# Optimization experiments

Hardware: AMD Instinct MI355X
Metric: run time of the kernel (lower is better)

## Reference

```python
import jax, jax.numpy as jnp
import numpy as np

V, E, H, L, B, T = 371, 512, 8, 8, 4, 1024
D = E // H
EPS = 1e-5


def setup_inputs() -> dict:
    key = jax.random.key(0)
    ks = jax.random.split(key, 7)
    s = 0.02
    return {
        "idx": jax.random.randint(ks[0], (B, T), 0, V),
        "wte": jax.random.normal(ks[1], (V, E), jnp.float32) * s,   # tied with lm_head
        "wpe": jax.random.normal(ks[2], (T, E), jnp.float32) * s,
        "c_attn_w": jax.random.normal(ks[3], (L, E, 3 * E), jnp.float32) * s,
        "c_proj_w": jax.random.normal(ks[4], (L, E, E), jnp.float32) * s,
        "fc_w": jax.random.normal(ks[5], (L, E, 4 * E), jnp.float32) * s,
        "fc_proj_w": jax.random.normal(ks[6], (L, 4 * E, E), jnp.float32) * s,
        "ln1_w": jnp.ones((L, E), jnp.float32),
        "ln2_w": jnp.ones((L, E), jnp.float32),
        "lnf_w": jnp.ones((E,), jnp.float32),
    }


def _ln(x, w):
    m = jnp.mean(x, axis=-1, keepdims=True)
    v = jnp.mean((x - m) ** 2, axis=-1, keepdims=True)
    return (x - m) * jax.lax.rsqrt(v + EPS) * w


def reference(idx, wte, wpe, c_attn_w, c_proj_w, fc_w, fc_proj_w, ln1_w, ln2_w, lnf_w):
    mask = jnp.tril(jnp.ones((T, T), bool))  # causal mask, as in the registered buffer
    scale = 1.0 / np.sqrt(D)

    x0 = wte[idx] + wpe[None, :T]  # [B,T,E]

    def block(x, p):
        aw, pw, l1, l2, fw, fpw = p
        h = _ln(x, l1)
        qkv = h @ aw                                   # [B,T,3E]
        q, k, v = jnp.split(qkv, 3, axis=-1)
        q = q.reshape(B, T, H, D)
        k = k.reshape(B, T, H, D)
        v = v.reshape(B, T, H, D)
        att = jnp.einsum("bqhd,bkhd->bhqk", q, k) * scale  # full TxT scores (faithful)
        att = jnp.where(mask[None, None], att, -jnp.inf)
        att = jax.nn.softmax(att, axis=-1)
        y = jnp.einsum("bhqk,bkhd->bqhd", att, v).reshape(B, T, E)
        x = x + y @ pw
        h = _ln(x, l2)
        x = x + jax.nn.gelu(h @ fw, approximate=False) @ fpw
        return x, None

    x, _ = jax.lax.scan(block, x0, (c_attn_w, c_proj_w, ln1_w, ln2_w, fc_w, fc_proj_w))
    x = _ln(x, lnf_w)
    logits = x @ wte.T  # weight tying: lm_head.weight = wte.weight
    return logits
```

## Files before the change

### kernel.cpp

```cpp
#include <hip/hip_runtime.h>


#define VOCAB 371
#define VPAD  384
#define EMB   512
#define NH    8
#define NL    8
#define TS    1024
#define NTOK  4096
#define NEG_INF (-1e30f)

typedef unsigned short ushort_t;
typedef __attribute__((ext_vector_type(8))) short short8;
typedef __attribute__((ext_vector_type(4))) float f32x4;

__device__ inline float bf2f(ushort_t b) {
    unsigned int u = ((unsigned int)b) << 16;
    float f; __builtin_memcpy(&f, &u, 4); return f;
}
__device__ inline ushort_t f2bf(float f) {
    unsigned int u; __builtin_memcpy(&u, &f, 4);
    u = (u + 0x7fff + ((u >> 16) & 1)) >> 16;
    return (ushort_t)u;
}

__global__ __launch_bounds__(64) void detect_k(const ushort_t* __restrict__ w,
        int* __restrict__ flag)
{
    int i = threadIdx.x;
    float v = bf2f(w[2 * i]);
    bool ok = (__builtin_fabsf(v) <= 4.0f);
    unsigned long long m = __ballot(ok);
    if (i == 0) flag[0] = (__popcll(m) >= 56) ? 1 : 0;
}

__global__ __launch_bounds__(256) void sentinel_k(ushort_t* __restrict__ out, int n)
{
    int i = blockIdx.x * 256 + threadIdx.x;
    if (i < n) out[i] = 0x447A;
}

__global__ __launch_bounds__(256) void embed_k(const int* __restrict__ idx,
        const void* __restrict__ wte, const void* __restrict__ wpe,
        float* __restrict__ x, const int* __restrict__ flag)
{
    int n = blockIdx.x, tid = threadIdx.x;
    int t = n & (TS - 1);
    int v = idx[n];
    size_t o = (size_t)n * EMB;
    float a0, a1, b0, b1;
    if (*flag) {
        const ushort_t* te = (const ushort_t*)wte; const ushort_t* pe = (const ushort_t*)wpe;
        a0 = bf2f(te[v * EMB + tid]); a1 = bf2f(te[v * EMB + 256 + tid]);
        b0 = bf2f(pe[t * EMB + tid]); b1 = bf2f(pe[t * EMB + 256 + tid]);
    } else {
        const float* te = (const float*)wte; const float* pe = (const float*)wpe;
        a0 = te[v * EMB + tid]; a1 = te[v * EMB + 256 + tid];
        b0 = pe[t * EMB + tid]; b1 = pe[t * EMB + 256 + tid];
    }
    x[o + tid] = a0 + b0;
    x[o + 256 + tid] = a1 + b1;
}

__global__ __launch_bounds__(256) void ln_k(const float* __restrict__ x,
        const void* __restrict__ w, long woff, ushort_t* __restrict__ out,
        const int* __restrict__ flag)
{
    const int row = blockIdx.x * 4 + (threadIdx.x >> 6);
    const int lane = threadIdx.x & 63;
    const float* xr = x + (size_t)row * EMB + lane * 8;
    float4 f0 = *(const float4*)xr;
    float4 f1 = *(const float4*)(xr + 4);
    float v[8] = {f0.x, f0.y, f0.z, f0.w, f1.x, f1.y, f1.z, f1.w};
    float s = ((v[0] + v[1]) + (v[2] + v[3])) + ((v[4] + v[5]) + (v[6] + v[7]));
#pragma unroll
    for (int off = 32; off > 0; off >>= 1) s += __shfl_xor(s, off, 64);
    float mean = s * (1.0f / EMB);
    float s2 = 0.f;
#pragma unroll
    for (int j = 0; j < 8; ++j) { v[j] -= mean; s2 += v[j] * v[j]; }
#pragma unroll
    for (int off = 32; off > 0; off >>= 1) s2 += __shfl_xor(s2, off, 64);
    float rs = rsqrtf(s2 * (1.0f / EMB) + 1e-5f);
    float g[8];
    if (*flag) {
        const ushort_t* wb = (const ushort_t*)w + woff + lane * 8;
        ushort_t tmp[8];
        *(uint4*)tmp = *(const uint4*)wb;
#pragma unroll
        for (int j = 0; j < 8; ++j) g[j] = bf2f(tmp[j]);
    } else {
        const float* wf = (const float*)w + woff + lane * 8;
        float4 g0 = *(const float4*)wf;
        float4 g1 = *(const float4*)(wf + 4);
        g[0] = g0.x; g[1] = g0.y; g[2] = g0.z; g[3] = g0.w;
        g[4] = g1.x; g[5] = g1.y; g[6] = g1.z; g[7] = g1.w;
    }
    ushort_t ob[8];
#pragma unroll
    for (int j = 0; j < 8; ++j) ob[j] = f2bf(v[j] * rs * g[j]);
    *(uint4*)(out + (size_t)row * EMB + lane * 8) = *(uint4*)ob;
}

__global__ __launch_bounds__(256) void wtrans_k(const void* __restrict__ aw,
        const void* __restrict__ pw, const void* __restrict__ fw,
        const void* __restrict__ fpw, long l, ushort_t* __restrict__ wbuf,
        const int* __restrict__ flag)
{
    __shared__ float tile[64][65];
    const int isbf = *flag;
    long lay = (l < 0) ? (long)blockIdx.z : l;
    ushort_t* obase = wbuf + ((l < 0) ? (size_t)blockIdx.z * 3145728 : 0);
    int t = blockIdx.x;
    const void* src; ushort_t* dst; int Kw, Nw; long ioff;
    if (t < 192)      { src = aw;  dst = obase;           Kw = 512;  Nw = 1536; ioff = lay * 512L * 1536; }
    else if (t < 256) { t -= 192; src = pw;  dst = obase + 786432;  Kw = 512;  Nw = 512;  ioff = lay * 512L * 512; }
    else if (t < 512) { t -= 256; src = fw;  dst = obase + 1048576; Kw = 512;  Nw = 2048; ioff = lay * 512L * 2048; }
    else              { t -= 512; src = fpw; dst = obase + 2097152; Kw = 2048; Nw = 512;  ioff = lay * 2048L * 512; }
    int tn = Nw >> 6;
    int n0 = (t % tn) * 64, k0 = (t / tn) * 64;
    const int r = threadIdx.x >> 2, cq = (threadIdx.x & 3) * 16;
    size_t ii = ioff + (size_t)(k0 + r) * Nw + n0 + cq;
    if (isbf) {
        const ushort_t* sb = (const ushort_t*)src + ii;
        ushort_t tmp[16];
        *(uint4*)tmp = *(const uint4*)sb;
        *(uint4*)(tmp + 8) = *(const uint4*)(sb + 8);
#pragma unroll
        for (int j = 0; j < 16; ++j) tile[r][cq + j] = bf2f(tmp[j]);
    } else {
        const float* sf = (const float*)src + ii;
        *(float4*)&tile[r][cq]      = *(const float4*)sf;
        *(float4*)&tile[r][cq + 4]  = *(const float4*)(sf + 4);
        *(float4*)&tile[r][cq + 8]  = *(const float4*)(sf + 8);
        *(float4*)&tile[r][cq + 12] = *(const float4*)(sf + 12);
    }
    __syncthreads();
    const int kc = (threadIdx.x & 7) * 8;
#pragma unroll
    for (int j = 0; j < 2; ++j) {
        const int n = (threadIdx.x >> 3) + j * 32;
        unsigned pk[4];
#pragma unroll
        for (int i = 0; i < 4; ++i) {
            unsigned lo = f2bf(tile[kc + 2 * i][n]);
            unsigned hi = f2bf(tile[kc + 2 * i + 1][n]);
            pk[i] = lo | (hi << 16);
        }
        *(uint4*)(dst + (size_t)(n0 + n) * Kw + k0 + kc) = *(uint4*)pk;
    }
}

__global__ __launch_bounds__(256) void wconv_k(const void* __restrict__ in,
        ushort_t* __restrict__ out, int n, int nreal, const int* __restrict__ flag)
{
    int i = blockIdx.x * 256 + threadIdx.x;
    if (i >= n) return;
    ushort_t v = 0;
    if (i < nreal) v = (*flag) ? ((const ushort_t*)in)[i] : f2bf(((const float*)in)[i]);
    out[i] = v;
}

__global__ __launch_bounds__(256) void gemm_wide(const ushort_t* __restrict__ A,
        const ushort_t* __restrict__ Bt, int M, int N, int K,
        float* __restrict__ outF, ushort_t* __restrict__ outB,
        const float* __restrict__ res, int act)
{
    __shared__ ushort_t Al[128 * 72];
    __shared__ ushort_t Bl[64 * 72];
    const int tid = threadIdx.x;
    const int wave = tid >> 6, lane = tid & 63;
    const int quad = lane >> 4, l16 = lane & 15;
    const int m0 = blockIdx.y * 128, n0 = blockIdx.x * 64;
    const int ar = tid >> 1, ac = (tid & 1) * 32;
    const int br = tid >> 2, bc = (tid & 3) * 16;
    const ushort_t* Ag = A + (size_t)(m0 + ar) * K + ac;
    const ushort_t* Bg = Bt + (size_t)(n0 + br) * K + bc;
    f32x4 acc[2][4] = {};
    uint4 a0 = *(const uint4*)(Ag);
    uint4 a1 = *(const uint4*)(Ag + 8);
    uint4 a2 = *(const uint4*)(Ag + 16);
    uint4 a3 = *(const uint4*)(Ag + 24);
    uint4 b0 = *(const uint4*)(Bg);
    uint4 b1 = *(const uint4*)(Bg + 8);
    for (int k0 = 0; k0 < K; k0 += 64) {
        __syncthreads();
        *(uint4*)&Al[ar * 72 + ac]      = a0;
        *(uint4*)&Al[ar * 72 + ac + 8]  = a1;
        *(uint4*)&Al[ar * 72 + ac + 16] = a2;
        *(uint4*)&Al[ar * 72 + ac + 24] = a3;
        *(uint4*)&Bl[br * 72 + bc]     = b0;
        *(uint4*)&Bl[br * 72 + bc + 8] = b1;
        __syncthreads();
        if (k0 + 64 < K) {
            a0 = *(const uint4*)(Ag + k0 + 64);
            a1 = *(const uint4*)(Ag + k0 + 72);
            a2 = *(const uint4*)(Ag + k0 + 80);
            a3 = *(const uint4*)(Ag + k0 + 88);
            b0 = *(const uint4*)(Bg + k0 + 64);
            b1 = *(const uint4*)(Bg + k0 + 72);
        }
#pragma unroll
        for (int ks = 0; ks < 2; ++ks) {
            short8 af[2], bf[4];
#pragma unroll
            for (int mi = 0; mi < 2; ++mi)
                af[mi] = *(const short8*)&Al[(wave * 32 + mi * 16 + l16) * 72 + ks * 32 + quad * 8];
#pragma unroll
            for (int ni = 0; ni < 4; ++ni)
                bf[ni] = *(const short8*)&Bl[(ni * 16 + l16) * 72 + ks * 32 + quad * 8];
#pragma unroll
            for (int mi = 0; mi < 2; ++mi)
#pragma unroll
                for (int ni = 0; ni < 4; ++ni)
                    acc[mi][ni] = __builtin_amdgcn_mfma_f32_16x16x32_bf16(
                            af[mi], bf[ni], acc[mi][ni], 0, 0, 0);
        }
    }
#pragma unroll
    for (int mi = 0; mi < 2; ++mi) {
        const int rowb = m0 + wave * 32 + mi * 16 + quad * 4;
#pragma unroll
        for (int ni = 0; ni < 4; ++ni) {
            const int col = n0 + ni * 16 + l16;
#pragma unroll
            for (int r = 0; r < 4; ++r) {
                size_t o = (size_t)(rowb + r) * N + col;
                float v = acc[mi][ni][r];
                if (res) v += res[o];
                if (act) v = 0.5f * v * (1.0f + erff(v * 0.70710678118f));
                if (outF) outF[o] = v;
                else      outB[o] = f2bf(v);
            }
        }
    }
}

__global__ __launch_bounds__(256) void gemm_nt(const ushort_t* __restrict__ A,
        const ushort_t* __restrict__ Bt, int M, int N, int K,
        float* __restrict__ outF, ushort_t* __restrict__ outB, void* __restrict__ outD,
        const float* __restrict__ res, int act, const int* __restrict__ flag)
{
    __shared__ ushort_t Al[64 * 72];
    __shared__ ushort_t Bl[64 * 72];
    const int isbf = *flag;
    const int tid = threadIdx.x;
    const int wave = tid >> 6, lane = tid & 63;
    const int quad = lane >> 4, l16 = lane & 15;
    const int m0 = blockIdx.y * 64, n0 = blockIdx.x * 64;
    const int sr = tid >> 2, sc = (tid & 3) * 16;
    const bool bok = (n0 + sr) < N;
    const ushort_t* Ag = A + (size_t)(m0 + sr) * K + sc;
    const ushort_t* Bg = Bt + (size_t)(n0 + sr) * K + sc;
    f32x4 acc[4] = {};
    uint4 a0 = *(const uint4*)(Ag);
    uint4 a1 = *(const uint4*)(Ag + 8);
    uint4 b0 = make_uint4(0, 0, 0, 0), b1 = make_uint4(0, 0, 0, 0);
    if (bok) { b0 = *(const uint4*)(Bg); b1 = *(const uint4*)(Bg + 8); }
    for (int k0 = 0; k0 < K; k0 += 64) {
        __syncthreads();
        *(uint4*)&Al[sr * 72 + sc] = a0; *(uint4*)&Al[sr * 72 + sc + 8] = a1;
        *(uint4*)&Bl[sr * 72 + sc] = b0; *(uint4*)&Bl[sr * 72 + sc + 8] = b1;
        __syncthreads();
        if (k0 + 64 < K) {
            a0 = *(const uint4*)(Ag + k0 + 64);
            a1 = *(const uint4*)(Ag + k0 + 72);
            if (bok) {
                b0 = *(const uint4*)(Bg + k0 + 64);
                b1 = *(const uint4*)(Bg + k0 + 72);
            }
        }
#pragma unroll
        for (int kc = 0; kc < 2; ++kc) {
            short8 af = *(const short8*)&Al[(wave * 16 + l16) * 72 + kc * 32 + quad * 8];
#pragma unroll
            for (int nt = 0; nt < 4; ++nt) {
                short8 bf = *(const short8*)&Bl[(nt * 16 + l16) * 72 + kc * 32 + quad * 8];
                acc[nt] = __builtin_amdgcn_mfma_f32_16x16x32_bf16(af, bf, acc[nt], 0, 0, 0);
            }
        }
    }
    const int mb = m0 + wave * 16 + quad * 4;
#pragma unroll
    for (int nt = 0; nt < 4; ++nt) {
        int nn = n0 + nt * 16 + l16;
        if (nn >= N) continue;
#pragma unroll
        for (int r = 0; r < 4; ++r) {
            size_t o = (size_t)(mb + r) * N + nn;
            float v = acc[nt][r];
            if (res) v += res[o];
            if (act) v = 0.5f * v * (1.0f + erff(v * 0.70710678118f));
            if (outF)      outF[o] = v;
            else if (outB) outB[o] = f2bf(v);
            else if (isbf) ((ushort_t*)outD)[o] = f2bf(v);
            else           ((float*)outD)[o] = v;
        }
    }
}

__global__ __launch_bounds__(256) void gemm_k(const ushort_t* __restrict__ A,
        const void* __restrict__ B, long boff, int M, int N, int K, int bt,
        float* __restrict__ outF, ushort_t* __restrict__ outB, void* __restrict__ outD,
        const float* __restrict__ res, int act, const int* __restrict__ flag)
{
    __shared__ ushort_t Al[64 * 40];
    __shared__ ushort_t Bl[64 * 40];
    const int isbf = *flag;
    const int tid = threadIdx.x;
    const int wave = tid >> 6, lane = tid & 63;
    const int quad = lane >> 4, l16 = lane & 15;
    const int m0 = blockIdx.y * 64, n0 = blockIdx.x * 64;
    const int sr = tid >> 2, sc = (tid & 3) * 8;
    const int kr = tid >> 3, nc = (tid & 7) * 8;
    f32x4 acc[4] = {};
    const bool bok = (n0 + sr) < N;
    const ushort_t* Ag = A + (size_t)(m0 + sr) * K + sc;
    const ushort_t* Bb = (const ushort_t*)B + boff;
    const float*    Bf = (const float*)B + boff;
    const size_t i1 = (size_t)(n0 + sr) * K + sc;
    const size_t i0 = (size_t)kr * N + n0 + nc;
    for (int k0 = 0; k0 < K; k0 += 32) {
        uint4 av = *(const uint4*)(Ag + k0);
        ushort_t b8[8] = {0, 0, 0, 0, 0, 0, 0, 0};
        size_t bi = bt ? (i1 + k0) : (i0 + (size_t)k0 * N);
        if (!bt || bok) {
            if (isbf) *(uint4*)b8 = *(const uint4*)(Bb + bi);
            else {
                float4 f0 = *(const float4*)(Bf + bi);
                float4 f1 = *(const float4*)(Bf + bi + 4);
                b8[0] = f2bf(f0.x); b8[1] = f2bf(f0.y); b8[2] = f2bf(f0.z); b8[3] = f2bf(f0.w);
                b8[4] = f2bf(f1.x); b8[5] = f2bf(f1.y); b8[6] = f2bf(f1.z); b8[7] = f2bf(f1.w);
            }
        }
        __syncthreads();
        *(uint4*)&Al[sr * 40 + sc] = av;
        if (bt) *(uint4*)&Bl[sr * 40 + sc] = *(uint4*)b8;
        else {
#pragma unroll
            for (int i = 0; i < 8; ++i) Bl[(nc + i) * 40 + kr] = b8[i];
        }
        __syncthreads();
        short8 af = *(const short8*)&Al[(wave * 16 + l16) * 40 + quad * 8];
#pragma unroll
        for (int nt = 0; nt < 4; ++nt) {
            short8 bf = *(const short8*)&Bl[(nt * 16 + l16) * 40 + quad * 8];
            acc[nt] = __builtin_amdgcn_mfma_f32_16x16x32_bf16(af, bf, acc[nt], 0, 0, 0);
        }
    }
    const int mb = m0 + wave * 16 + quad * 4;
#pragma unroll
    for (int nt = 0; nt < 4; ++nt) {
        int nn = n0 + nt * 16 + l16;
        if (nn >= N) continue;
#pragma unroll
        for (int r = 0; r < 4; ++r) {
            size_t o = (size_t)(mb + r) * N + nn;
            float v = acc[nt][r];
            if (res) v += res[o];
            if (act) v = 0.5f * v * (1.0f + erff(v * 0.70710678118f));
            if (outF)      outF[o] = v;
            else if (outB) outB[o] = f2bf(v);
            else if (isbf) ((ushort_t*)outD)[o] = f2bf(v);
            else           ((float*)outD)[o] = v;
        }
    }
}

__global__ __launch_bounds__(256) void attn_k(const ushort_t* __restrict__ qkv,
        ushort_t* __restrict__ y)
{
    __shared__ ushort_t Kl[64 * 72];
    __shared__ ushort_t Vt[64 * 72];
    __shared__ ushort_t Pl[4][16 * 72];
    const int tid = threadIdx.x, wave = tid >> 6, lane = tid & 63;
    const int quad = lane >> 4, l16 = lane & 15;
    const int qt = (int)gridDim.x - 1 - blockIdx.x;
    const int b = blockIdx.y >> 3, h = blockIdx.y & 7;
    const int q0b = qt * 64;
    const int q0w = q0b + wave * 16;
    const size_t rstr = 3 * EMB;
    const ushort_t* qbase = qkv + ((size_t)(b * TS) + q0w + l16) * rstr + h * 64;
    short8 qf0, qf1;
    {
        ushort_t q0[8], q1[8];
        *(uint4*)q0 = *(const uint4*)(qbase + quad * 8);
        *(uint4*)q1 = *(const uint4*)(qbase + 32 + quad * 8);
#pragma unroll
        for (int i = 0; i < 8; ++i) {
            qf0[i] = (short)f2bf(bf2f(q0[i]) * 0.125f);
            qf1[i] = (short)f2bf(bf2f(q1[i]) * 0.125f);
        }
    }
    short8 onesf;
#pragma unroll
    for (int i = 0; i < 8; ++i) onesf[i] = (short)0x3F80;
    f32x4 O[4] = {};
    f32x4 lacc = {};
    const int sk = tid >> 2, sdc = (tid & 3) * 16;
    const int vp = tid >> 3, vdc = (tid & 7) * 8;
    const int vsh = 16 * ((tid & 7) & 3);
    const int vcol = (2 * vp + vsh) & 63;
    const ushort_t* kbase = qkv + ((size_t)(b * TS) + sk) * rstr + EMB + h * 64 + sdc;
    const ushort_t* vbase = qkv + ((size_t)(b * TS) + 2 * vp) * rstr + 2 * EMB + h * 64 + vdc;
    uint4 kv0 = *(const uint4*)(kbase);
    uint4 kv1 = *(const uint4*)(kbase + 8);
    uint4 vv0 = *(const uint4*)(vbase);
    uint4 vv1 = *(const uint4*)(vbase + rstr);
    for (int kt = 0; kt <= qt; ++kt) {
        __syncthreads();
        *(uint4*)&Kl[sk * 72 + sdc]     = kv0;
        *(uint4*)&Kl[sk * 72 + sdc + 8] = kv1;
        {
            ushort_t v0[8], v1[8];
            *(uint4*)v0 = vv0; *(uint4*)v1 = vv1;
#pragma unroll
            for (int i = 0; i < 8; ++i) {
                unsigned pk = (unsigned)v0[i] | ((unsigned)v1[i] << 16);
                *(unsigned*)&Vt[(vdc + i) * 72 + vcol] = pk;
            }
        }
        __syncthreads();
        if (kt < qt) {
            const size_t off = (size_t)(kt + 1) * 64 * rstr;
            kv0 = *(const uint4*)(kbase + off);
            kv1 = *(const uint4*)(kbase + off + 8);
            vv0 = *(const uint4*)(vbase + off);
            vv1 = *(const uint4*)(vbase + off + rstr);
        }
        if (kt < qt) {
            f32x4 S[4] = {};
#pragma unroll
            for (int nt = 0; nt < 4; ++nt) {
                short8 kf0 = *(const short8*)&Kl[(nt * 16 + l16) * 72 + quad * 8];
                short8 kf1 = *(const short8*)&Kl[(nt * 16 + l16) * 72 + 32 + quad * 8];
                S[nt] = __builtin_amdgcn_mfma_f32_16x16x32_bf16(qf0, kf0, S[nt], 0, 0, 0);
                S[nt] = __builtin_amdgcn_mfma_f32_16x16x32_bf16(qf1, kf1, S[nt], 0, 0, 0);
            }
#pragma unroll
            for (int nt = 0; nt < 4; ++nt)
#pragma unroll
                for (int r = 0; r < 4; ++r)
                    Pl[wave][(quad * 4 + r) * 72 + nt * 16 + l16] = f2bf(__expf(S[nt][r]));
        } else {
            f32x4 S[4] = {};
#pragma unroll
            for (int nt = 0; nt < 4; ++nt) {
                if (nt > wave) continue;
                short8 kf0 = *(const short8*)&Kl[(nt * 16 + l16) * 72 + quad * 8];
                short8 kf1 = *(const short8*)&Kl[(nt * 16 + l16) * 72 + 32 + quad * 8];
                S[nt] = __builtin_amdgcn_mfma_f32_16x16x32_bf16(qf0, kf0, S[nt], 0, 0, 0);
                S[nt] = __builtin_amdgcn_mfma_f32_16x16x32_bf16(qf1, kf1, S[nt], 0, 0, 0);
            }
#pragma unroll
            for (int nt = 0; nt < 4; ++nt)
#pragma unroll
                for (int r = 0; r < 4; ++r) {
                    bool live = (nt < wave) || (nt == wave && l16 <= quad * 4 + r);
                    float p = live ? __expf(S[nt][r]) : 0.f;
                    Pl[wave][(quad * 4 + r) * 72 + nt * 16 + l16] = f2bf(p);
                }
        }
#pragma unroll
        for (int kc = 0; kc < 2; ++kc) {
            short8 pf = *(const short8*)&Pl[wave][l16 * 72 + kc * 32 + quad * 8];
            lacc = __builtin_amdgcn_mfma_f32_16x16x32_bf16(pf, onesf, lacc, 0, 0, 0);
#pragma unroll
            for (int dt = 0; dt < 4; ++dt) {
                int d = dt * 16 + l16;
                int sh = ((2 * dt + (l16 >> 3)) & 3) * 16;
                int col = (kc * 32 + quad * 8 + sh) & 63;
                short8 vf = *(const short8*)&Vt[d * 72 + col];
                O[dt] = __builtin_amdgcn_mfma_f32_16x16x32_bf16(pf, vf, O[dt], 0, 0, 0);
            }
        }
    }
#pragma unroll
    for (int dt = 0; dt < 4; ++dt)
#pragma unroll
        for (int r = 0; r < 4; ++r) {
            int q = q0w + quad * 4 + r;
            float v = O[dt][r] / lacc[r];
            y[((size_t)(b * TS) + q) * EMB + h * 64 + dt * 16 + l16] = f2bf(v);
        }
}

extern "C" void kernel_launch(void* const* d_in, const int* in_sizes, int n_in,
                              void* d_out, int out_size, void* d_ws, size_t ws_size,
                              hipStream_t stream)
{
    const int*  idx    = (const int*)d_in[0];
    const void* wte    = d_in[1];
    const void* wpe    = d_in[2];
    const void* attn_w = d_in[3];
    const void* proj_w = d_in[4];
    const void* fc_w   = d_in[5];
    const void* fcp_w  = d_in[6];
    const void* ln1_w  = d_in[7];
    const void* ln2_w  = d_in[8];
    const void* lnf_w  = d_in[9];

    const size_t sz_xw    = (size_t)NTOK * EMB * 4;
    const size_t sz_hbf   = (size_t)NTOK * EMB * 2;
    const size_t sz_big   = (size_t)NTOK * 2048 * 2;
    const size_t sz_wteb  = (size_t)VPAD * EMB * 2;
    const size_t sz_wbuf1 = (size_t)3145728 * 2;
    const size_t need_legacy = 256 + sz_xw + sz_hbf + sz_big;
    const size_t need_fast   = need_legacy + sz_wteb + sz_wbuf1;
    const size_t need_all    = need_legacy + sz_wteb + NL * sz_wbuf1;

    if (ws_size < need_legacy) {
        sentinel_k<<<(out_size + 255) / 256, 256, 0, stream>>>((ushort_t*)d_out, out_size);
        return;
    }
    int* flag = (int*)d_ws;
    char* p = (char*)d_ws + 256;
    float*    xw  = (float*)p;    p += sz_xw;
    ushort_t* hbf = (ushort_t*)p; p += sz_hbf;
    ushort_t* big = (ushort_t*)p; p += sz_big;

    detect_k<<<1, 64, 0, stream>>>((const ushort_t*)wte, flag);
    embed_k<<<NTOK, 256, 0, stream>>>(idx, wte, wpe, xw, flag);

    if (ws_size >= need_fast) {
        ushort_t* wteb = (ushort_t*)p; p += sz_wteb;
        ushort_t* wbuf = (ushort_t*)p;
        const bool allw = (ws_size >= need_all);
        wconv_k<<<(VPAD * EMB + 255) / 256, 256, 0, stream>>>(wte, wteb,
                VPAD * EMB, VOCAB * EMB, flag);
        if (allw)
            wtrans_k<<<dim3(768, 1, NL), 256, 0, stream>>>(attn_w, proj_w, fc_w, fcp_w,
                    -1, wbuf, flag);
        for (int l = 0; l < NL; ++l) {
            ushort_t* wb = allw ? (wbuf + (size_t)l * 3145728) : wbuf;
            if (!allw)
                wtrans_k<<<dim3(768, 1, 1), 256, 0, stream>>>(attn_w, proj_w, fc_w, fcp_w,
                        (long)l, wbuf, flag);
            ln_k<<<NTOK / 4, 256, 0, stream>>>(xw, ln1_w, (long)l * EMB, hbf, flag);
            gemm_wide<<<dim3(24, 32), 256, 0, stream>>>(hbf, wb,
                    NTOK, 1536, 512, nullptr, big, nullptr, 0);
            attn_k<<<dim3(16, 32), 256, 0, stream>>>(big, hbf);
            gemm_nt<<<dim3(8, 64), 256, 0, stream>>>(hbf, wb + 786432,
                    NTOK, 512, 512, xw, nullptr, nullptr, xw, 0, flag);
            ln_k<<<NTOK / 4, 256, 0, stream>>>(xw, ln2_w, (long)l * EMB, hbf, flag);
            gemm_wide<<<dim3(32, 32), 256, 0, stream>>>(hbf, wb + 1048576,
                    NTOK, 2048, 512, nullptr, big, nullptr, 1 );
            gemm_nt<<<dim3(8, 64), 256, 0, stream>>>(big, wb + 2097152,
                    NTOK, 512, 2048, xw, nullptr, nullptr, xw, 0, flag);
        }
        ln_k<<<NTOK / 4, 256, 0, stream>>>(xw, lnf_w, 0, hbf, flag);
        gemm_nt<<<dim3(6, 64), 256, 0, stream>>>(hbf, wteb,
                NTOK, VOCAB, 512, nullptr, nullptr, d_out, nullptr, 0, flag);
    } else {
        for (int l = 0; l < NL; ++l) {
            ln_k<<<NTOK / 4, 256, 0, stream>>>(xw, ln1_w, (long)l * EMB, hbf, flag);
            gemm_k<<<dim3(24, 64), 256, 0, stream>>>(hbf, attn_w, (long)l * 512 * 1536,
                    NTOK, 1536, 512, 0, nullptr, big, nullptr, nullptr, 0, flag);
            attn_k<<<dim3(16, 32), 256, 0, stream>>>(big, hbf);
            gemm_k<<<dim3(8, 64), 256, 0, stream>>>(hbf, proj_w, (long)l * 512 * 512,
                    NTOK, 512, 512, 0, xw, nullptr, nullptr, xw, 0, flag);
            ln_k<<<NTOK / 4, 256, 0, stream>>>(xw, ln2_w, (long)l * EMB, hbf, flag);
            gemm_k<<<dim3(32, 64), 256, 0, stream>>>(hbf, fc_w, (long)l * 512 * 2048,
                    NTOK, 2048, 512, 0, nullptr, big, nullptr, nullptr, 1, flag);
            gemm_k<<<dim3(8, 64), 256, 0, stream>>>(big, fcp_w, (long)l * 2048 * 512,
                    NTOK, 512, 2048, 0, xw, nullptr, nullptr, xw, 0, flag);
        }
        ln_k<<<NTOK / 4, 256, 0, stream>>>(xw, lnf_w, 0, hbf, flag);
        gemm_k<<<dim3(6, 64), 256, 0, stream>>>(hbf, wte, 0,
                NTOK, VOCAB, 512, 1, nullptr, nullptr, d_out, nullptr, 0, flag);
    }
}
```

Measured before the change: 1.109 ms.

## Keep attention probabilities in registers via transposed MFMA, drop LDS staging

The attention kernel now computes S^T by swapping the MFMA operands, so each lane already holds the probabilities it needs as the A/B fragment for the P·V MFMA. The per-wave LDS buffer for P and the ones-vector MFMA row sum are removed. The row sum is instead accumulated in registers and reduced with two cross-lane shuffles. The V-transpose column permutation is changed to match the new key ordering, and outputs are written as packed 8-byte stores. This removes LDS round trips and some MFMAs per tile, at the cost of relying on a subtle permutation whose correctness depends on the fragment layout.

```diff
diff --git a/kernel.cpp b/kernel.cpp
--- a/kernel.cpp
+++ b/kernel.cpp
@@ -372,7 +372,6 @@
 {
     __shared__ ushort_t Kl[64 * 72];
     __shared__ ushort_t Vt[64 * 72];
-    __shared__ ushort_t Pl[4][16 * 72];
     const int tid = threadIdx.x, wave = tid >> 6, lane = tid & 63;
     const int quad = lane >> 4, l16 = lane & 15;
     const int qt = (int)gridDim.x - 1 - blockIdx.x;
@@ -392,15 +391,14 @@
             qf1[i] = (short)f2bf(bf2f(q1[i]) * 0.125f);
         }
     }
-    short8 onesf;
-#pragma unroll
-    for (int i = 0; i < 8; ++i) onesf[i] = (short)0x3F80;
     f32x4 O[4] = {};
-    f32x4 lacc = {};
+    float lsum = 0.f;
     const int sk = tid >> 2, sdc = (tid & 3) * 16;
     const int vp = tid >> 3, vdc = (tid & 7) * 8;
     const int vsh = 16 * ((tid & 7) & 3);
-    const int vcol = (2 * vp + vsh) & 63;
+    const int p0 = ((vp >> 4) << 5) | (((vp >> 1) & 3) << 3)
+                 | (((vp >> 3) & 1) << 2) | ((vp & 1) << 1);
+    const int vcol = (p0 + vsh) & 63;
     const ushort_t* kbase = qkv + ((size_t)(b * TS) + sk) * rstr + EMB + h * 64 + sdc;
     const ushort_t* vbase = qkv + ((size_t)(b * TS) + 2 * vp) * rstr + 2 * EMB + h * 64 + vdc;
     uint4 kv0 = *(const uint4*)(kbase);
@@ -428,61 +426,55 @@
             vv0 = *(const uint4*)(vbase + off);
             vv1 = *(const uint4*)(vbase + off + rstr);
         }
-        if (kt < qt) {
-            f32x4 S[4] = {};
-#pragma unroll
-            for (int nt = 0; nt < 4; ++nt) {
-                short8 kf0 = *(const short8*)&Kl[(nt * 16 + l16) * 72 + quad * 8];
-                short8 kf1 = *(const short8*)&Kl[(nt * 16 + l16) * 72 + 32 + quad * 8];
-                S[nt] = __builtin_amdgcn_mfma_f32_16x16x32_bf16(qf0, kf0, S[nt], 0, 0, 0);
-                S[nt] = __builtin_amdgcn_mfma_f32_16x16x32_bf16(qf1, kf1, S[nt], 0, 0, 0);
-            }
-#pragma unroll
-            for (int nt = 0; nt < 4; ++nt)
-#pragma unroll
-                for (int r = 0; r < 4; ++r)
-                    Pl[wave][(quad * 4 + r) * 72 + nt * 16 + l16] = f2bf(__expf(S[nt][r]));
-        } else {
-            f32x4 S[4] = {};
-#pragma unroll
-            for (int nt = 0; nt < 4; ++nt) {
-                if (nt > wave) continue;
-                short8 kf0 = *(const short8*)&Kl[(nt * 16 + l16) * 72 + quad * 8];
-                short8 kf1 = *(const short8*)&Kl[(nt * 16 + l16) * 72 + 32 + quad * 8];
-                S[nt] = __builtin_amdgcn_mfma_f32_16x16x32_bf16(qf0, kf0, S[nt], 0, 0, 0);
-                S[nt] = __builtin_amdgcn_mfma_f32_16x16x32_bf16(qf1, kf1, S[nt], 0, 0, 0);
-            }
-#pragma unroll
-            for (int nt = 0; nt < 4; ++nt)
-#pragma unroll
-                for (int r = 0; r < 4; ++r) {
-                    bool live = (nt < wave) || (nt == wave && l16 <= quad * 4 + r);
-                    float p = live ? __expf(S[nt][r]) : 0.f;
-                    Pl[wave][(quad * 4 + r) * 72 + nt * 16 + l16] = f2bf(p);
-                }
+        const bool diag = (kt == qt);
+        f32x4 S[4] = {};
+#pragma unroll
+        for (int nt = 0; nt < 4; ++nt) {
+            if (diag && nt > wave) continue;
+            short8 kf0 = *(const short8*)&Kl[(nt * 16 + l16) * 72 + quad * 8];
+            short8 kf1 = *(const short8*)&Kl[(nt * 16 + l16) * 72 + 32 + quad * 8];
+            S[nt] = __builtin_amdgcn_mfma_f32_16x16x32_bf16(kf0, qf0, S[nt], 0, 0, 0);
+            S[nt] = __builtin_amdgcn_mfma_f32_16x16x32_bf16(kf1, qf1, S[nt], 0, 0, 0);
+        }
+        unsigned pk[4][2];
+#pragma unroll
+        for (int nt = 0; nt < 4; ++nt) {
+            float p[4];
+#pragma unroll
+            for (int r = 0; r < 4; ++r) {
+                bool live = !diag || (nt * 16 + quad * 4 + r <= wave * 16 + l16);
+                p[r] = live ? __expf(S[nt][r]) : 0.f;
+                lsum += p[r];
+            }
+            pk[nt][0] = (unsigned)f2bf(p[0]) | ((unsigned)f2bf(p[1]) << 16);
+            pk[nt][1] = (unsigned)f2bf(p[2]) | ((unsigned)f2bf(p[3]) << 16);
         }
 #pragma unroll
         for (int kc = 0; kc < 2; ++kc) {
-            short8 pf = *(const short8*)&Pl[wave][l16 * 72 + kc * 32 + quad * 8];
-            lacc = __builtin_amdgcn_mfma_f32_16x16x32_bf16(pf, onesf, lacc, 0, 0, 0);
+            unsigned pw[4] = {pk[2 * kc][0], pk[2 * kc][1],
+                              pk[2 * kc + 1][0], pk[2 * kc + 1][1]};
+            short8 pf = *(const short8*)pw;
 #pragma unroll
             for (int dt = 0; dt < 4; ++dt) {
                 int d = dt * 16 + l16;
                 int sh = ((2 * dt + (l16 >> 3)) & 3) * 16;
                 int col = (kc * 32 + quad * 8 + sh) & 63;
                 short8 vf = *(const short8*)&Vt[d * 72 + col];
-                O[dt] = __builtin_amdgcn_mfma_f32_16x16x32_bf16(pf, vf, O[dt], 0, 0, 0);
-            }
-        }
-    }
-#pragma unroll
-    for (int dt = 0; dt < 4; ++dt)
-#pragma unroll
-        for (int r = 0; r < 4; ++r) {
-            int q = q0w + quad * 4 + r;
-            float v = O[dt][r] / lacc[r];
-            y[((size_t)(b * TS) + q) * EMB + h * 64 + dt * 16 + l16] = f2bf(v);
-        }
+                O[dt] = __builtin_amdgcn_mfma_f32_16x16x32_bf16(vf, pf, O[dt], 0, 0, 0);
+            }
+        }
+    }
+    lsum += __shfl_xor(lsum, 16, 64);
+    lsum += __shfl_xor(lsum, 32, 64);
+    const float inv = 1.0f / lsum;
+    ushort_t* yb = y + ((size_t)(b * TS) + q0w + l16) * EMB + h * 64 + quad * 4;
+#pragma unroll
+    for (int dt = 0; dt < 4; ++dt) {
+        unsigned ow[2];
+        ow[0] = (unsigned)f2bf(O[dt][0] * inv) | ((unsigned)f2bf(O[dt][1] * inv) << 16);
+        ow[1] = (unsigned)f2bf(O[dt][2] * inv) | ((unsigned)f2bf(O[dt][3] * inv) << 16);
+        *(uint2*)(yb + dt * 16) = *(uint2*)ow;
+    }
 }
 
 extern "C" void kernel_launch(void* const* d_in, const int* in_sizes, int n_in,
```

Result: faster. 1.083 ms (-2.3%).
